# Performance work log

Measured on AMD Instinct MI355X. Metric: run time of the kernel, lower is better.

## Reference

```python
import jax, jax.numpy as jnp
import numpy as np

N_NODES = 50000
N_EDGES = 800000
NFEAT = 512
NHID = 64
NHEADS = 8
NCLASS = 40
ALPHA = 0.2  # LeakyReLU slope
EPS = 1e-16  # guards isolated-node division


def setup_inputs() -> dict:
    key = jax.random.key(0)
    k = jax.random.split(key, 6)
    x = jax.random.normal(k[0], (N_NODES, NFEAT), dtype=jnp.float32)
    W_heads = jax.random.normal(k[1], (NHEADS, NFEAT, NHID), dtype=jnp.float32) * 0.05
    a_heads = jax.random.normal(k[2], (NHEADS, 2 * NHID), dtype=jnp.float32) * 0.05
    W_out = jax.random.normal(k[3], (NHEADS * NHID, NCLASS), dtype=jnp.float32) * 0.05
    a_out = jax.random.normal(k[4], (2 * NCLASS,), dtype=jnp.float32) * 0.05
    edge_index = jax.random.randint(k[5], (2, N_EDGES), 0, N_NODES, dtype=jnp.int32)
    return {"x": x, "W_heads": W_heads, "a_heads": a_heads,
            "W_out": W_out, "a_out": a_out, "edge_index": edge_index}


def _gat_layer(x, W, a, row, col, concat):
    # pyGAT sparse layer: h = xW; e_ij = exp(-LeakyReLU(a^T [h_i || h_j]));
    # out_i = sum_j e_ij h_j / sum_j e_ij   (aggregate into row, gather from col)
    D = W.shape[1]
    h = x @ W                                            # [N, D]
    score = h[row] @ a[:D] + h[col] @ a[D:]              # [E]
    e = jnp.exp(-jax.nn.leaky_relu(score, ALPHA))        # [E]
    num = jax.ops.segment_sum(e[:, None] * h[col], row, num_segments=x.shape[0])  # [N, D]
    den = jax.ops.segment_sum(e, row, num_segments=x.shape[0])                    # [N]
    out = num / (den[:, None] + EPS)
    return jax.nn.elu(out) if concat else out


def reference(x, W_heads, a_heads, W_out, a_out, edge_index):
    # dropout layers are identity in eval mode (training=False)
    row, col = edge_index[0], edge_index[1]
    heads = jax.vmap(lambda W, a: _gat_layer(x, W, a, row, col, True))(W_heads, a_heads)
    # [H, N, D] -> [N, H*D] (concat along feature dim, head-major like torch.cat)
    hcat = jnp.transpose(heads, (1, 0, 2)).reshape(x.shape[0], -1)
    return _gat_layer(hcat, W_out, a_out, row, col, False)  # [N, NCLASS]
```

## Files before the change

kernel.cpp:

```cpp
#include <hip/hip_runtime.h>
#include <hip/hip_bf16.h>

#define N_NODES 50000
#define N_EDGES 800000
#define NFEAT   512
#define NHID    64
#define NHEADS  8
#define NCLASS  40
#define HD      (NHEADS*NHID)
#define ALPHA   0.2f
#define EPS_F   1e-16f
#define NCHUNK  ((N_NODES + 255)/256)

typedef __attribute__((ext_vector_type(8))) short short8;
typedef __attribute__((ext_vector_type(4))) float floatx4;

__device__ __forceinline__ float bf2f(unsigned short u) {
    union { unsigned int i; float f; } v; v.i = ((unsigned int)u) << 16; return v.f;
}
__device__ __forceinline__ unsigned short f2bf(float f) {
    union { __hip_bfloat16 h; unsigned short u; } cv;
    cv.h = __float2bfloat16(f);
    return cv.u;
}

__global__ void prep(const float* __restrict__ Wh, unsigned short* __restrict__ Wrb,
                     const float* __restrict__ Wo, unsigned short* __restrict__ Wob,
                     int* __restrict__ deg) {
    int idx = blockIdx.x*256 + threadIdx.x;
    if (idx >= 512*512) return;
    if (idx < N_NODES) deg[idx] = 0;
    {
        int n = idx >> 9, k = idx & 511;
        int hd = n >> 6, d = n & 63;
        Wrb[idx] = f2bf(Wh[(size_t)hd*NFEAT*NHID + (size_t)k*NHID + d]);
    }
    if (idx < 64*512) {
        int n = idx >> 9, k = idx & 511;
        float v = (n < NCLASS) ? Wo[(size_t)k*NCLASS + n] : 0.f;
        Wob[idx] = f2bf(v);
    }
}

__global__ __launch_bounds__(256) void mfma_gemm1(const float* __restrict__ A,
                                                  const unsigned short* __restrict__ Bbf,
                                                  const float* __restrict__ a_heads,
                                                  unsigned short* __restrict__ H1p,
                                                  float* __restrict__ srcdot,
                                                  float* __restrict__ dstdot, int M) {
    int id = blockIdx.x;
    int rb = (id >> 5)*8 + (id & 7);
    int cb = (id >> 3) & 3;
    int row0 = rb * 128, col0 = cb * 128;
    if (row0 >= M) return;

    __shared__ short Asl[128*40];
    __shared__ short Bsl[128*40];
    int tid  = threadIdx.x;
    int wid  = tid >> 6, lane = tid & 63;
    int lrow = lane & 15, quad = lane >> 4;
    int wm = wid & 1, wn = wid >> 1;

    int sr[2], sk[2];
#pragma unroll
    for (int it = 0; it < 2; ++it) {
        int q = tid + it*256;
        sr[it] = q >> 2; sk[it] = (q & 3) * 8;
    }
    int arow[2];
#pragma unroll
    for (int it = 0; it < 2; ++it) {
        int ar = row0 + sr[it];
        arow[it] = ar < M ? ar : M - 1;
    }

    floatx4 acc[4][4];
#pragma unroll
    for (int mm = 0; mm < 4; mm++)
#pragma unroll
        for (int nn = 0; nn < 4; nn++) acc[mm][nn] = (floatx4){0.f,0.f,0.f,0.f};

    float4 fa[2][2];
    short8 fb[2];
#pragma unroll
    for (int it = 0; it < 2; ++it) {
        const float* src = A + (size_t)arow[it]*512 + sk[it];
        fa[it][0] = *(const float4*)src;
        fa[it][1] = *(const float4*)(src + 4);
        fb[it] = *(const short8*)(Bbf + (size_t)(col0 + sr[it])*512 + sk[it]);
    }

    for (int k0 = 0; k0 < 512; k0 += 32) {
#pragma unroll
        for (int it = 0; it < 2; ++it) {
            short8 h;
            h[0] = (short)f2bf(fa[it][0].x); h[1] = (short)f2bf(fa[it][0].y);
            h[2] = (short)f2bf(fa[it][0].z); h[3] = (short)f2bf(fa[it][0].w);
            h[4] = (short)f2bf(fa[it][1].x); h[5] = (short)f2bf(fa[it][1].y);
            h[6] = (short)f2bf(fa[it][1].z); h[7] = (short)f2bf(fa[it][1].w);
            *(short8*)(&Asl[sr[it]*40 + sk[it]]) = h;
            *(short8*)(&Bsl[sr[it]*40 + sk[it]]) = fb[it];
        }
        __syncthreads();
        if (k0 + 32 < 512) {
            int kn = k0 + 32;
#pragma unroll
            for (int it = 0; it < 2; ++it) {
                const float* src = A + (size_t)arow[it]*512 + kn + sk[it];
                fa[it][0] = *(const float4*)src;
                fa[it][1] = *(const float4*)(src + 4);
                fb[it] = *(const short8*)(Bbf + (size_t)(col0 + sr[it])*512 + kn + sk[it]);
            }
        }
        short8 af[4], bfr[4];
#pragma unroll
        for (int mm = 0; mm < 4; ++mm)
            af[mm] = *(const short8*)(&Asl[(wm*64 + mm*16 + lrow)*40 + quad*8]);
#pragma unroll
        for (int nn = 0; nn < 4; ++nn)
            bfr[nn] = *(const short8*)(&Bsl[(wn*64 + nn*16 + lrow)*40 + quad*8]);
#pragma unroll
        for (int mm = 0; mm < 4; ++mm)
#pragma unroll
            for (int nn = 0; nn < 4; ++nn)
                acc[mm][nn] = __builtin_amdgcn_mfma_f32_16x16x32_bf16(
                    af[mm], bfr[nn], acc[mm][nn], 0, 0, 0);
        __syncthreads();
    }

    {
        int head = (col0 >> 6) + wn;
        float a0v[4], a1v[4];
#pragma unroll
        for (int nn = 0; nn < 4; ++nn) {
            a0v[nn] = a_heads[head*128 + nn*16 + lrow];
            a1v[nn] = a_heads[head*128 + 64 + nn*16 + lrow];
        }
#pragma unroll
        for (int mm = 0; mm < 4; ++mm) {
#pragma unroll
            for (int r = 0; r < 4; ++r) {
                float s0 = 0.f, s1 = 0.f;
#pragma unroll
                for (int nn = 0; nn < 4; ++nn) {
                    float v = acc[mm][nn][r];
                    s0 = fmaf(v, a0v[nn], s0);
                    s1 = fmaf(v, a1v[nn], s1);
                }
#pragma unroll
                for (int off = 1; off < 16; off <<= 1) {
                    s0 += __shfl_xor(s0, off, 64);
                    s1 += __shfl_xor(s1, off, 64);
                }
                int grow = row0 + wm*64 + mm*16 + quad*4 + r;
                if (lrow == 0 && grow < M) {
                    srcdot[(size_t)grow*8 + head] = s0;
                    dstdot[(size_t)grow*8 + head] = s1;
                }
            }
        }
    }

#pragma unroll
    for (int mm = 0; mm < 4; ++mm) {
        int rbase = row0 + wm*64 + mm*16 + quad*4;
#pragma unroll
        for (int nn = 0; nn < 4; ++nn) {
            int c = col0 + wn*64 + nn*16 + lrow;
            int off = (c & 63)*8 + (c >> 6);
#pragma unroll
            for (int r = 0; r < 4; ++r) {
                int grow = rbase + r;
                if (grow < M)
                    H1p[(size_t)grow*512 + off] = f2bf(acc[mm][nn][r]);
            }
        }
    }
}

__global__ __launch_bounds__(256) void mfma_gemm2(const unsigned short* __restrict__ Abf,
                                                  const unsigned short* __restrict__ Bbf,
                                                  const float* __restrict__ a_out,
                                                  float* __restrict__ H2p,
                                                  float* __restrict__ src2,
                                                  float* __restrict__ dst2, int M) {
    __shared__ short Asl[256*40];
    __shared__ short Bsl[64*40];
    int tid  = threadIdx.x;
    int wid  = tid >> 6, lane = tid & 63;
    int lrow = lane & 15, quad = lane >> 4;
    int row0 = blockIdx.x * 256;

    floatx4 acc[4][4];
#pragma unroll
    for (int mm = 0; mm < 4; mm++)
#pragma unroll
        for (int nn = 0; nn < 4; nn++) acc[mm][nn] = (floatx4){0.f,0.f,0.f,0.f};

    for (int k0 = 0; k0 < 512; k0 += 32) {
#pragma unroll
        for (int it = 0; it < 4; ++it) {
            int q  = tid + it*256;
            int r  = q >> 2, kk = (q & 3) * 8;
            int ar = row0 + r; ar = ar < M ? ar : M - 1;
            *(short8*)(&Asl[r*40 + kk]) =
                *(const short8*)(Abf + (size_t)ar*512 + k0 + kk);
        }
        {
            int r = tid >> 2, kk = (tid & 3) * 8;
            *(short8*)(&Bsl[r*40 + kk]) =
                *(const short8*)(Bbf + (size_t)r*512 + k0 + kk);
        }
        __syncthreads();
        short8 af[4], bfr[4];
#pragma unroll
        for (int mm = 0; mm < 4; ++mm)
            af[mm] = *(const short8*)(&Asl[(wid*64 + mm*16 + lrow)*40 + quad*8]);
#pragma unroll
        for (int nn = 0; nn < 4; ++nn)
            bfr[nn] = *(const short8*)(&Bsl[(nn*16 + lrow)*40 + quad*8]);
#pragma unroll
        for (int mm = 0; mm < 4; ++mm)
#pragma unroll
            for (int nn = 0; nn < 4; ++nn)
                acc[mm][nn] = __builtin_amdgcn_mfma_f32_16x16x32_bf16(
                    af[mm], bfr[nn], acc[mm][nn], 0, 0, 0);
        __syncthreads();
    }

    {
        float a0v[4], a1v[4];
#pragma unroll
        for (int nn = 0; nn < 4; ++nn) {
            int c = nn*16 + lrow;
            a0v[nn] = c < NCLASS ? a_out[c] : 0.f;
            a1v[nn] = c < NCLASS ? a_out[NCLASS + c] : 0.f;
        }
#pragma unroll
        for (int mm = 0; mm < 4; ++mm) {
#pragma unroll
            for (int r = 0; r < 4; ++r) {
                float s0 = 0.f, s1 = 0.f;
#pragma unroll
                for (int nn = 0; nn < 4; ++nn) {
                    float v = acc[mm][nn][r];
                    s0 = fmaf(v, a0v[nn], s0);
                    s1 = fmaf(v, a1v[nn], s1);
                }
#pragma unroll
                for (int off = 1; off < 16; off <<= 1) {
                    s0 += __shfl_xor(s0, off, 64);
                    s1 += __shfl_xor(s1, off, 64);
                }
                int grow = row0 + wid*64 + mm*16 + quad*4 + r;
                if (lrow == 0 && grow < M) {
                    src2[grow] = s0;
                    dst2[grow] = s1;
                }
            }
        }
    }

#pragma unroll
    for (int mm = 0; mm < 4; ++mm) {
        int rbase = row0 + wid*64 + mm*16 + quad*4;
#pragma unroll
        for (int nn = 0; nn < 4; ++nn) {
            int c = nn*16 + lrow;
#pragma unroll
            for (int r = 0; r < 4; ++r) {
                int grow = rbase + r;
                if (grow < M)
                    H2p[(size_t)grow*64 + c] = acc[mm][nn][r];
            }
        }
    }
}

__global__ void histk(const int* __restrict__ row, int* __restrict__ deg) {
    int e = blockIdx.x*256 + threadIdx.x;
    if (e < N_EDGES) atomicAdd(&deg[row[e]], 1);
}
__global__ void scanA(const int* __restrict__ deg, int* __restrict__ row_ptr,
                      int* __restrict__ chunk_tot) {
    __shared__ int s[256];
    int t = threadIdx.x;
    int idx = blockIdx.x*256 + t;
    int v = (idx < N_NODES) ? deg[idx] : 0;
    s[t] = v;
    __syncthreads();
#pragma unroll
    for (int off = 1; off < 256; off <<= 1) {
        int x = (t >= off) ? s[t-off] : 0;
        __syncthreads();
        s[t] += x;
        __syncthreads();
    }
    if (idx < N_NODES) row_ptr[idx] = s[t] - v;
    if (t == 255) chunk_tot[blockIdx.x] = s[t];
}
__global__ void scanB(const int* __restrict__ chunk_tot, int* __restrict__ chunk_off,
                      int* __restrict__ row_ptr) {
    __shared__ int s[256];
    int t = threadIdx.x;
    int v = (t < NCHUNK) ? chunk_tot[t] : 0;
    s[t] = v;
    __syncthreads();
#pragma unroll
    for (int off = 1; off < 256; off <<= 1) {
        int x = (t >= off) ? s[t-off] : 0;
        __syncthreads();
        s[t] += x;
        __syncthreads();
    }
    if (t < NCHUNK) chunk_off[t] = s[t] - v;
    if (t == 255) row_ptr[N_NODES] = s[t];
}
__global__ void scanC(const int* __restrict__ chunk_off, int* __restrict__ row_ptr,
                      int* __restrict__ cursor) {
    int idx = blockIdx.x*256 + threadIdx.x;
    if (idx < N_NODES) {
        int rp = row_ptr[idx] + chunk_off[idx >> 8];
        row_ptr[idx] = rp;
        cursor[idx] = rp;
    }
}

__global__ void fillk_w1(const int* __restrict__ row, const int* __restrict__ col,
                         const float* __restrict__ srcdot, const float* __restrict__ dstdot,
                         int* __restrict__ cursor, int* __restrict__ csr_col,
                         float* __restrict__ Wcsr) {
    int e = blockIdx.x*256 + threadIdx.x;
    if (e >= N_EDGES) return;
    int r = row[e], c = col[e];
    int pos = atomicAdd(&cursor[r], 1);
    csr_col[pos] = c;
    float4 sa = *(const float4*)(srcdot + (size_t)r*8);
    float4 sb = *(const float4*)(srcdot + (size_t)r*8 + 4);
    float4 da = *(const float4*)(dstdot + (size_t)c*8);
    float4 db = *(const float4*)(dstdot + (size_t)c*8 + 4);
    float s[8] = {sa.x+da.x, sa.y+da.y, sa.z+da.z, sa.w+da.w,
                  sb.x+db.x, sb.y+db.y, sb.z+db.z, sb.w+db.w};
    float o[8];
#pragma unroll
    for (int j = 0; j < 8; j++) {
        float lr = s[j] > 0.f ? s[j] : ALPHA*s[j];
        o[j] = __expf(-lr);
    }
    *(float4*)(Wcsr + (size_t)pos*8)     = make_float4(o[0], o[1], o[2], o[3]);
    *(float4*)(Wcsr + (size_t)pos*8 + 4) = make_float4(o[4], o[5], o[6], o[7]);
}

__global__ __launch_bounds__(256) void agg1(const unsigned short* __restrict__ H1p,
                                            const float* __restrict__ Wcsr,
                                            const int* __restrict__ row_ptr,
                                            const int* __restrict__ csr_col,
                                            unsigned short* __restrict__ hcatb) {
    int wave = (blockIdx.x*256 + threadIdx.x) >> 6;
    int lane = threadIdx.x & 63;
    if (wave >= N_NODES) return;
    int start = row_ptr[wave], end = row_ptr[wave+1];
    float acc[8], den[8];
#pragma unroll
    for (int j = 0; j < 8; j++) { acc[j] = 0.f; den[j] = 0.f; }

    int k = start;
    for (; k + 4 <= end; k += 4) {
        int c0 = csr_col[k],   c1 = csr_col[k+1];
        int c2 = csr_col[k+2], c3 = csr_col[k+3];
        short8 hv0 = *(const short8*)(H1p + (size_t)c0*512 + lane*8);
        short8 hv1 = *(const short8*)(H1p + (size_t)c1*512 + lane*8);
        short8 hv2 = *(const short8*)(H1p + (size_t)c2*512 + lane*8);
        short8 hv3 = *(const short8*)(H1p + (size_t)c3*512 + lane*8);
        float4 wv[8];
#pragma unroll
        for (int q = 0; q < 8; q++)
            wv[q] = *(const float4*)(Wcsr + (size_t)k*8 + q*4);
        const float* w0 = (const float*)&wv[0];
        const float* w1 = (const float*)&wv[2];
        const float* w2 = (const float*)&wv[4];
        const float* w3 = (const float*)&wv[6];
#pragma unroll
        for (int j = 0; j < 8; j++) {
            den[j] += (w0[j] + w1[j]) + (w2[j] + w3[j]);
            acc[j] = fmaf(w0[j], bf2f((unsigned short)hv0[j]), acc[j]);
            acc[j] = fmaf(w1[j], bf2f((unsigned short)hv1[j]), acc[j]);
            acc[j] = fmaf(w2[j], bf2f((unsigned short)hv2[j]), acc[j]);
            acc[j] = fmaf(w3[j], bf2f((unsigned short)hv3[j]), acc[j]);
        }
    }
    for (; k < end; ++k) {
        int c = csr_col[k];
        float4 wa = *(const float4*)(Wcsr + (size_t)k*8);
        float4 wb = *(const float4*)(Wcsr + (size_t)k*8 + 4);
        short8 hv = *(const short8*)(H1p + (size_t)c*512 + lane*8);
        float w[8] = {wa.x, wa.y, wa.z, wa.w, wb.x, wb.y, wb.z, wb.w};
#pragma unroll
        for (int j = 0; j < 8; j++) {
            den[j] += w[j];
            acc[j] = fmaf(w[j], bf2f((unsigned short)hv[j]), acc[j]);
        }
    }
#pragma unroll
    for (int j = 0; j < 8; j++) {
        float o = acc[j] / (den[j] + EPS_F);
        o = o > 0.f ? o : (__expf(o) - 1.f);
        hcatb[(size_t)wave*HD + j*64 + lane] = f2bf(o);
    }
}

__global__ __launch_bounds__(256) void agg2(const float* __restrict__ H2p,
                                            const float* __restrict__ src2,
                                            const float* __restrict__ dst2,
                                            const int* __restrict__ row_ptr,
                                            const int* __restrict__ csr_col,
                                            float* __restrict__ out) {
    int wave = (blockIdx.x*256 + threadIdx.x) >> 6;
    int lane = threadIdx.x & 63;
    if (wave >= N_NODES) return;
    int start = row_ptr[wave], end = row_ptr[wave+1];
    int deg = end - start;
    float s2i = src2[wave];
    int l = lane < NCLASS ? lane : 0;
    float acc = 0.f, den = 0.f;

    int colreg = 0;
    if (deg > 0) colreg = csr_col[start + (lane < deg ? lane : deg - 1)];

#define AG2_G1(T, H, IDX) do { \
    int cg_ = __builtin_amdgcn_readlane(colreg, (IDX)); \
    T = dst2[cg_]; \
    H = H2p[(size_t)cg_*64 + l]; \
} while(0)
#define AG2_C1(T, H) do { \
    float t_ = s2i + (T); \
    t_ = t_ > 0.f ? t_ : ALPHA*t_; \
    float w_ = __expf(-t_); \
    den += w_; acc = fmaf(w_, (H), acc); \
} while(0)
#define AG2_G8(T0,T1,T2,T3,T4,T5,T6,T7,H0,H1,H2,H3,H4,H5,H6,H7,BASE) do { \
    AG2_G1(T0,H0,(BASE));   AG2_G1(T1,H1,(BASE)+1); \
    AG2_G1(T2,H2,(BASE)+2); AG2_G1(T3,H3,(BASE)+3); \
    AG2_G1(T4,H4,(BASE)+4); AG2_G1(T5,H5,(BASE)+5); \
    AG2_G1(T6,H6,(BASE)+6); AG2_G1(T7,H7,(BASE)+7); \
} while(0)
#define AG2_C8(T0,T1,T2,T3,T4,T5,T6,T7,H0,H1,H2,H3,H4,H5,H6,H7) do { \
    AG2_C1(T0,H0); AG2_C1(T1,H1); AG2_C1(T2,H2); AG2_C1(T3,H3); \
    AG2_C1(T4,H4); AG2_C1(T5,H5); AG2_C1(T6,H6); AG2_C1(T7,H7); \
} while(0)

    int lim = deg < 64 ? deg : 64;
    int nb = lim >> 3;
    int k = start;
    float ta0,ta1,ta2,ta3,ta4,ta5,ta6,ta7, ga0,ga1,ga2,ga3,ga4,ga5,ga6,ga7;
    float tb0,tb1,tb2,tb3,tb4,tb5,tb6,tb7, gb0,gb1,gb2,gb3,gb4,gb5,gb6,gb7;
    if (nb > 0) {
        AG2_G8(ta0,ta1,ta2,ta3,ta4,ta5,ta6,ta7, ga0,ga1,ga2,ga3,ga4,ga5,ga6,ga7, 0);
        int b = 1;
        for (; b + 1 < nb; b += 2) {
            AG2_G8(tb0,tb1,tb2,tb3,tb4,tb5,tb6,tb7, gb0,gb1,gb2,gb3,gb4,gb5,gb6,gb7, b*8);
            AG2_C8(ta0,ta1,ta2,ta3,ta4,ta5,ta6,ta7, ga0,ga1,ga2,ga3,ga4,ga5,ga6,ga7);
            AG2_G8(ta0,ta1,ta2,ta3,ta4,ta5,ta6,ta7, ga0,ga1,ga2,ga3,ga4,ga5,ga6,ga7, (b+1)*8);
            AG2_C8(tb0,tb1,tb2,tb3,tb4,tb5,tb6,tb7, gb0,gb1,gb2,gb3,gb4,gb5,gb6,gb7);
        }
        if (b < nb) {
            AG2_G8(tb0,tb1,tb2,tb3,tb4,tb5,tb6,tb7, gb0,gb1,gb2,gb3,gb4,gb5,gb6,gb7, b*8);
            AG2_C8(ta0,ta1,ta2,ta3,ta4,ta5,ta6,ta7, ga0,ga1,ga2,ga3,ga4,ga5,ga6,ga7);
            AG2_C8(tb0,tb1,tb2,tb3,tb4,tb5,tb6,tb7, gb0,gb1,gb2,gb3,gb4,gb5,gb6,gb7);
        } else {
            AG2_C8(ta0,ta1,ta2,ta3,ta4,ta5,ta6,ta7, ga0,ga1,ga2,ga3,ga4,ga5,ga6,ga7);
        }
        k = start + nb*8;
    }
    for (; k < end; ++k) {
        int c_ = (k - start < 64) ? __builtin_amdgcn_readlane(colreg, k - start)
                                  : csr_col[k];
        float t = dst2[c_];
        float h = H2p[(size_t)c_*64 + l];
        AG2_C1(t, h);
    }
#undef AG2_G1
#undef AG2_C1
#undef AG2_G8
#undef AG2_C8

    if (lane < NCLASS)
        out[(size_t)wave*NCLASS + lane] = acc / (den + EPS_F);
}

extern "C" void kernel_launch(void* const* d_in, const int* in_sizes, int n_in,
                              void* d_out, int out_size, void* d_ws, size_t ws_size,
                              hipStream_t stream) {
    const float* x       = (const float*)d_in[0];
    const float* W_heads = (const float*)d_in[1];
    const float* a_heads = (const float*)d_in[2];
    const float* W_out   = (const float*)d_in[3];
    const float* a_out   = (const float*)d_in[4];
    const int*   ei      = (const int*)d_in[5];
    const int*   row     = ei;
    const int*   col     = ei + N_EDGES;
    float* out = (float*)d_out;

    char* ws = (char*)d_ws;
    size_t off = 0;
    auto alloc = [&](size_t bytes) {
        char* p = ws + off;
        off = (off + bytes + 255) & ~(size_t)255;
        return p;
    };
    unsigned short* Wrb   = (unsigned short*)alloc((size_t)512*512*2);
    unsigned short* Wob   = (unsigned short*)alloc((size_t)64*512*2);
    unsigned short* H1p   = (unsigned short*)alloc((size_t)N_NODES*HD*2);
    unsigned short* hcatb = (unsigned short*)alloc((size_t)N_NODES*HD*2);
    float* srcdot  = (float*)alloc((size_t)N_NODES*NHEADS*4);
    float* dstdot  = (float*)alloc((size_t)N_NODES*NHEADS*4);
    float* Wcsr    = (float*)alloc((size_t)N_EDGES*NHEADS*4);
    int*   deg     = (int*)alloc((size_t)N_NODES*4);
    int*   row_ptr = (int*)alloc((size_t)(N_NODES+1)*4);
    int*   cursor  = (int*)alloc((size_t)N_NODES*4);
    int*   ctot    = (int*)alloc(256*4);
    int*   coff    = (int*)alloc(256*4);
    int*   csr_col = (int*)alloc((size_t)N_EDGES*4);
    float* H2p     = (float*)alloc((size_t)N_NODES*64*4);
    float* src2    = (float*)alloc((size_t)N_NODES*4);
    float* dst2    = (float*)alloc((size_t)N_NODES*4);
    (void)ws_size;

    const int EB = (N_EDGES + 255)/256;
    const int WB = (N_NODES*64 + 255)/256;

    prep<<<(512*512 + 255)/256, 256, 0, stream>>>(W_heads, Wrb, W_out, Wob, deg);
    {
        int rtiles = (N_NODES + 127)/128;
        int nblk = ((rtiles + 7)/8) * 32;
        mfma_gemm1<<<nblk, 256, 0, stream>>>(x, Wrb, a_heads, H1p,
                                             srcdot, dstdot, N_NODES);
    }

    histk<<<EB, 256, 0, stream>>>(row, deg);
    scanA<<<NCHUNK, 256, 0, stream>>>(deg, row_ptr, ctot);
    scanB<<<1, 256, 0, stream>>>(ctot, coff, row_ptr);
    scanC<<<NCHUNK, 256, 0, stream>>>(coff, row_ptr, cursor);
    fillk_w1<<<EB, 256, 0, stream>>>(row, col, srcdot, dstdot, cursor,
                                     csr_col, Wcsr);

    agg1<<<WB, 256, 0, stream>>>(H1p, Wcsr, row_ptr, csr_col, hcatb);

    mfma_gemm2<<<(N_NODES + 255)/256, 256, 0, stream>>>(hcatb, Wob, a_out,
                                                        H2p, src2, dst2, N_NODES);
    agg2<<<WB, 256, 0, stream>>>(H2p, src2, dst2, row_ptr, csr_col, out);
}
```

Measured before the change: 510.1 us.

## Use 512-thread blocks with smaller per-wave tiles in both MFMA GEMMs

Both GEMM kernels now launch 512 threads (8 waves) per block. Each wave owns a smaller accumulator tile (2x4 MFMA tiles in gemm1, 1x4 in gemm2), and each thread stages one global load per k-step. gemm2 also shrinks its row tile from 256 to 128 and adds register prefetch of the next k-slice, so global loads overlap the MFMA work. The goal is lower register pressure, higher occupancy and better latency hiding, at the cost of more B-fragment LDS reads per MFMA and more blocks.

```diff
diff --git a/kernel.cpp b/kernel.cpp
--- a/kernel.cpp
+++ b/kernel.cpp
@@ -42,7 +42,7 @@
     }
 }
 
-__global__ __launch_bounds__(256) void mfma_gemm1(const float* __restrict__ A,
+__global__ __launch_bounds__(512, 4) void mfma_gemm1(const float* __restrict__ A,
                                                   const unsigned short* __restrict__ Bbf,
                                                   const float* __restrict__ a_heads,
                                                   unsigned short* __restrict__ H1p,
@@ -59,68 +59,54 @@
     int tid  = threadIdx.x;
     int wid  = tid >> 6, lane = tid & 63;
     int lrow = lane & 15, quad = lane >> 4;
-    int wm = wid & 1, wn = wid >> 1;
-
-    int sr[2], sk[2];
-#pragma unroll
-    for (int it = 0; it < 2; ++it) {
-        int q = tid + it*256;
-        sr[it] = q >> 2; sk[it] = (q & 3) * 8;
-    }
-    int arow[2];
-#pragma unroll
-    for (int it = 0; it < 2; ++it) {
-        int ar = row0 + sr[it];
-        arow[it] = ar < M ? ar : M - 1;
-    }
-
-    floatx4 acc[4][4];
-#pragma unroll
-    for (int mm = 0; mm < 4; mm++)
+    int wm = wid >> 1, wn = wid & 1;
+
+    int sr = tid >> 2, sk = (tid & 3) * 8;
+    int ar = row0 + sr;
+    int arow = ar < M ? ar : M - 1;
+
+    floatx4 acc[2][4];
+#pragma unroll
+    for (int mm = 0; mm < 2; mm++)
 #pragma unroll
         for (int nn = 0; nn < 4; nn++) acc[mm][nn] = (floatx4){0.f,0.f,0.f,0.f};
 
-    float4 fa[2][2];
-    short8 fb[2];
-#pragma unroll
-    for (int it = 0; it < 2; ++it) {
-        const float* src = A + (size_t)arow[it]*512 + sk[it];
-        fa[it][0] = *(const float4*)src;
-        fa[it][1] = *(const float4*)(src + 4);
-        fb[it] = *(const short8*)(Bbf + (size_t)(col0 + sr[it])*512 + sk[it]);
+    float4 fa0, fa1;
+    short8 fb;
+    {
+        const float* src = A + (size_t)arow*512 + sk;
+        fa0 = *(const float4*)src;
+        fa1 = *(const float4*)(src + 4);
+        fb  = *(const short8*)(Bbf + (size_t)(col0 + sr)*512 + sk);
     }
 
     for (int k0 = 0; k0 < 512; k0 += 32) {
-#pragma unroll
-        for (int it = 0; it < 2; ++it) {
+        {
             short8 h;
-            h[0] = (short)f2bf(fa[it][0].x); h[1] = (short)f2bf(fa[it][0].y);
-            h[2] = (short)f2bf(fa[it][0].z); h[3] = (short)f2bf(fa[it][0].w);
-            h[4] = (short)f2bf(fa[it][1].x); h[5] = (short)f2bf(fa[it][1].y);
-            h[6] = (short)f2bf(fa[it][1].z); h[7] = (short)f2bf(fa[it][1].w);
-            *(short8*)(&Asl[sr[it]*40 + sk[it]]) = h;
-            *(short8*)(&Bsl[sr[it]*40 + sk[it]]) = fb[it];
+            h[0] = (short)f2bf(fa0.x); h[1] = (short)f2bf(fa0.y);
+            h[2] = (short)f2bf(fa0.z); h[3] = (short)f2bf(fa0.w);
+            h[4] = (short)f2bf(fa1.x); h[5] = (short)f2bf(fa1.y);
+            h[6] = (short)f2bf(fa1.z); h[7] = (short)f2bf(fa1.w);
+            *(short8*)(&Asl[sr*40 + sk]) = h;
+            *(short8*)(&Bsl[sr*40 + sk]) = fb;
         }
         __syncthreads();
         if (k0 + 32 < 512) {
             int kn = k0 + 32;
-#pragma unroll
-            for (int it = 0; it < 2; ++it) {
-                const float* src = A + (size_t)arow[it]*512 + kn + sk[it];
-                fa[it][0] = *(const float4*)src;
-                fa[it][1] = *(const float4*)(src + 4);
-                fb[it] = *(const short8*)(Bbf + (size_t)(col0 + sr[it])*512 + kn + sk[it]);
-            }
-        }
-        short8 af[4], bfr[4];
-#pragma unroll
-        for (int mm = 0; mm < 4; ++mm)
-            af[mm] = *(const short8*)(&Asl[(wm*64 + mm*16 + lrow)*40 + quad*8]);
+            const float* src = A + (size_t)arow*512 + kn + sk;
+            fa0 = *(const float4*)src;
+            fa1 = *(const float4*)(src + 4);
+            fb  = *(const short8*)(Bbf + (size_t)(col0 + sr)*512 + kn + sk);
+        }
+        short8 af[2], bfr[4];
+#pragma unroll
+        for (int mm = 0; mm < 2; ++mm)
+            af[mm] = *(const short8*)(&Asl[(wm*32 + mm*16 + lrow)*40 + quad*8]);
 #pragma unroll
         for (int nn = 0; nn < 4; ++nn)
             bfr[nn] = *(const short8*)(&Bsl[(wn*64 + nn*16 + lrow)*40 + quad*8]);
 #pragma unroll
-        for (int mm = 0; mm < 4; ++mm)
+        for (int mm = 0; mm < 2; ++mm)
 #pragma unroll
             for (int nn = 0; nn < 4; ++nn)
                 acc[mm][nn] = __builtin_amdgcn_mfma_f32_16x16x32_bf16(
@@ -137,7 +123,7 @@
             a1v[nn] = a_heads[head*128 + 64 + nn*16 + lrow];
         }
 #pragma unroll
-        for (int mm = 0; mm < 4; ++mm) {
+        for (int mm = 0; mm < 2; ++mm) {
 #pragma unroll
             for (int r = 0; r < 4; ++r) {
                 float s0 = 0.f, s1 = 0.f;
@@ -152,7 +138,7 @@
                     s0 += __shfl_xor(s0, off, 64);
                     s1 += __shfl_xor(s1, off, 64);
                 }
-                int grow = row0 + wm*64 + mm*16 + quad*4 + r;
+                int grow = row0 + wm*32 + mm*16 + quad*4 + r;
                 if (lrow == 0 && grow < M) {
                     srcdot[(size_t)grow*8 + head] = s0;
                     dstdot[(size_t)grow*8 + head] = s1;
@@ -162,8 +148,8 @@
     }
 
 #pragma unroll
-    for (int mm = 0; mm < 4; ++mm) {
-        int rbase = row0 + wm*64 + mm*16 + quad*4;
+    for (int mm = 0; mm < 2; ++mm) {
+        int rbase = row0 + wm*32 + mm*16 + quad*4;
 #pragma unroll
         for (int nn = 0; nn < 4; ++nn) {
             int c = col0 + wn*64 + nn*16 + lrow;
@@ -178,53 +164,53 @@
     }
 }
 
-__global__ __launch_bounds__(256) void mfma_gemm2(const unsigned short* __restrict__ Abf,
+__global__ __launch_bounds__(512, 4) void mfma_gemm2(const unsigned short* __restrict__ Abf,
                                                   const unsigned short* __restrict__ Bbf,
                                                   const float* __restrict__ a_out,
                                                   float* __restrict__ H2p,
                                                   float* __restrict__ src2,
                                                   float* __restrict__ dst2, int M) {
-    __shared__ short Asl[256*40];
+    __shared__ short Asl[128*40];
     __shared__ short Bsl[64*40];
     int tid  = threadIdx.x;
     int wid  = tid >> 6, lane = tid & 63;
     int lrow = lane & 15, quad = lane >> 4;
-    int row0 = blockIdx.x * 256;
-
-    floatx4 acc[4][4];
-#pragma unroll
-    for (int mm = 0; mm < 4; mm++)
-#pragma unroll
-        for (int nn = 0; nn < 4; nn++) acc[mm][nn] = (floatx4){0.f,0.f,0.f,0.f};
+    int row0 = blockIdx.x * 128;
+    if (row0 >= M) return;
+
+    int sr = tid >> 2, sk = (tid & 3) * 8;
+    int ar = row0 + sr; ar = ar < M ? ar : M - 1;
+    int sr2 = (tid & 255) >> 2, sk2 = (tid & 3) * 8;
+
+    floatx4 acc[4];
+#pragma unroll
+    for (int nn = 0; nn < 4; nn++) acc[nn] = (floatx4){0.f,0.f,0.f,0.f};
+
+    short8 fa, fbv;
+    fa = *(const short8*)(Abf + (size_t)ar*512 + sk);
+    if (tid < 256)
+        fbv = *(const short8*)(Bbf + (size_t)sr2*512 + sk2);
 
     for (int k0 = 0; k0 < 512; k0 += 32) {
-#pragma unroll
-        for (int it = 0; it < 4; ++it) {
-            int q  = tid + it*256;
-            int r  = q >> 2, kk = (q & 3) * 8;
-            int ar = row0 + r; ar = ar < M ? ar : M - 1;
-            *(short8*)(&Asl[r*40 + kk]) =
-                *(const short8*)(Abf + (size_t)ar*512 + k0 + kk);
-        }
-        {
-            int r = tid >> 2, kk = (tid & 3) * 8;
-            *(short8*)(&Bsl[r*40 + kk]) =
-                *(const short8*)(Bbf + (size_t)r*512 + k0 + kk);
-        }
-        __syncthreads();
-        short8 af[4], bfr[4];
-#pragma unroll
-        for (int mm = 0; mm < 4; ++mm)
-            af[mm] = *(const short8*)(&Asl[(wid*64 + mm*16 + lrow)*40 + quad*8]);
+        *(short8*)(&Asl[sr*40 + sk]) = fa;
+        if (tid < 256)
+            *(short8*)(&Bsl[sr2*40 + sk2]) = fbv;
+        __syncthreads();
+        if (k0 + 32 < 512) {
+            int kn = k0 + 32;
+            fa = *(const short8*)(Abf + (size_t)ar*512 + kn + sk);
+            if (tid < 256)
+                fbv = *(const short8*)(Bbf + (size_t)sr2*512 + kn + sk2);
+        }
+        short8 af, bfr[4];
+        af = *(const short8*)(&Asl[(wid*16 + lrow)*40 + quad*8]);
 #pragma unroll
         for (int nn = 0; nn < 4; ++nn)
             bfr[nn] = *(const short8*)(&Bsl[(nn*16 + lrow)*40 + quad*8]);
 #pragma unroll
-        for (int mm = 0; mm < 4; ++mm)
-#pragma unroll
-            for (int nn = 0; nn < 4; ++nn)
-                acc[mm][nn] = __builtin_amdgcn_mfma_f32_16x16x32_bf16(
-                    af[mm], bfr[nn], acc[mm][nn], 0, 0, 0);
+        for (int nn = 0; nn < 4; ++nn)
+            acc[nn] = __builtin_amdgcn_mfma_f32_16x16x32_bf16(
+                af, bfr[nn], acc[nn], 0, 0, 0);
         __syncthreads();
     }
 
@@ -237,42 +223,35 @@
             a1v[nn] = c < NCLASS ? a_out[NCLASS + c] : 0.f;
         }
 #pragma unroll
-        for (int mm = 0; mm < 4; ++mm) {
-#pragma unroll
-            for (int r = 0; r < 4; ++r) {
-                float s0 = 0.f, s1 = 0.f;
-#pragma unroll
-                for (int nn = 0; nn < 4; ++nn) {
-                    float v = acc[mm][nn][r];
-                    s0 = fmaf(v, a0v[nn], s0);
-                    s1 = fmaf(v, a1v[nn], s1);
-                }
-#pragma unroll
-                for (int off = 1; off < 16; off <<= 1) {
-                    s0 += __shfl_xor(s0, off, 64);
-                    s1 += __shfl_xor(s1, off, 64);
-                }
-                int grow = row0 + wid*64 + mm*16 + quad*4 + r;
-                if (lrow == 0 && grow < M) {
-                    src2[grow] = s0;
-                    dst2[grow] = s1;
-                }
+        for (int r = 0; r < 4; ++r) {
+            float s0 = 0.f, s1 = 0.f;
+#pragma unroll
+            for (int nn = 0; nn < 4; ++nn) {
+                float v = acc[nn][r];
+                s0 = fmaf(v, a0v[nn], s0);
+                s1 = fmaf(v, a1v[nn], s1);
             }
-        }
-    }
-
-#pragma unroll
-    for (int mm = 0; mm < 4; ++mm) {
-        int rbase = row0 + wid*64 + mm*16 + quad*4;
-#pragma unroll
-        for (int nn = 0; nn < 4; ++nn) {
-            int c = nn*16 + lrow;
-#pragma unroll
-            for (int r = 0; r < 4; ++r) {
-                int grow = rbase + r;
-                if (grow < M)
-                    H2p[(size_t)grow*64 + c] = acc[mm][nn][r];
+#pragma unroll
+            for (int off = 1; off < 16; off <<= 1) {
+                s0 += __shfl_xor(s0, off, 64);
+                s1 += __shfl_xor(s1, off, 64);
             }
+            int grow = row0 + wid*16 + quad*4 + r;
+            if (lrow == 0 && grow < M) {
+                src2[grow] = s0;
+                dst2[grow] = s1;
+            }
+        }
+    }
+
+#pragma unroll
+    for (int nn = 0; nn < 4; ++nn) {
+        int c = nn*16 + lrow;
+#pragma unroll
+        for (int r = 0; r < 4; ++r) {
+            int grow = row0 + wid*16 + quad*4 + r;
+            if (grow < M)
+                H2p[(size_t)grow*64 + c] = acc[nn][r];
         }
     }
 }
@@ -533,7 +512,7 @@
     {
         int rtiles = (N_NODES + 127)/128;
         int nblk = ((rtiles + 7)/8) * 32;
-        mfma_gemm1<<<nblk, 256, 0, stream>>>(x, Wrb, a_heads, H1p,
+        mfma_gemm1<<<nblk, 512, 0, stream>>>(x, Wrb, a_heads, H1p,
                                              srcdot, dstdot, N_NODES);
     }
 
@@ -546,7 +525,7 @@
 
     agg1<<<WB, 256, 0, stream>>>(H1p, Wcsr, row_ptr, csr_col, hcatb);
 
-    mfma_gemm2<<<(N_NODES + 255)/256, 256, 0, stream>>>(hcatb, Wob, a_out,
+    mfma_gemm2<<<(N_NODES + 127)/128, 512, 0, stream>>>(hcatb, Wob, a_out,
                                                         H2p, src2, dst2, N_NODES);
     agg2<<<WB, 256, 0, stream>>>(H2p, src2, dst2, row_ptr, csr_col, out);
 }
```

Measured after the change: 498.7 us. 2.2% less time.
